# Performance work log

Hardware: AMD Instinct MI355X
Metric: run time of the kernel (lower is better)

The kernel has to match this reference:

```python
import jax, jax.numpy as jnp
import numpy as np

N, E, B = 20000, 200000, 16
ND, ED, GD, HD, DOF = 64, 32, 32, 128, 6
PI = 3.14159265358979

def _hat(v):
    x, y, z = v[..., 0], v[..., 1], v[..., 2]
    O = jnp.zeros_like(x)
    return jnp.stack([jnp.stack([O, -z, y], -1),
                      jnp.stack([z, O, -x], -1),
                      jnp.stack([-y, x, O], -1)], -2)

def _so3_exp(phi):
    th2 = jnp.sum(phi * phi, -1, keepdims=True)
    th = jnp.sqrt(th2 + 1e-12)
    a = jnp.where(th < 1e-4, 1.0 - th2 / 6.0, jnp.sin(th) / th)
    b = jnp.where(th < 1e-4, 0.5 - th2 / 24.0, (1.0 - jnp.cos(th)) / th2)
    K = _hat(phi)
    I = jnp.eye(3, dtype=phi.dtype)
    return I + a[..., None] * K + b[..., None] * (K @ K)

def _se3_exp(rho, phi):
    # returns (R, t) of Exp([rho, phi]) with rotation part phi
    th2 = jnp.sum(phi * phi, -1, keepdims=True)
    th = jnp.sqrt(th2 + 1e-12)
    a = jnp.where(th < 1e-4, 1.0 - th2 / 6.0, jnp.sin(th) / th)
    b = jnp.where(th < 1e-4, 0.5 - th2 / 24.0, (1.0 - jnp.cos(th)) / th2)
    c = jnp.where(th < 1e-4, 1.0 / 6.0 - th2 / 120.0, (th - jnp.sin(th)) / (th2 * th))
    K = _hat(phi)
    KK = K @ K
    I = jnp.eye(3, dtype=phi.dtype)
    R = I + a[..., None] * K + b[..., None] * KK
    V = I + b[..., None] * K + c[..., None] * KK
    t = jnp.einsum('nij,nj->ni', V, rho)
    return R, t

def _comp(Ra, ta, Rb, tb):
    return Ra @ Rb, jnp.einsum('nij,nj->ni', Ra, tb) + ta

def _inv(R, t):
    Rt = jnp.swapaxes(R, -1, -2)
    return Rt, -jnp.einsum('nij,nj->ni', Rt, t)

def _vec(R, t):
    # flattened [R | t] 3x4 -> 12
    return jnp.concatenate([R, t[..., None]], -1).reshape(R.shape[0], 12)

def setup_inputs() -> dict:
    key = jax.random.key(0)
    ks = jax.random.split(key, 16)
    T_R = _so3_exp(0.5 * jax.random.normal(ks[0], (N, 3)))
    Tij_R = _so3_exp(0.5 * jax.random.normal(ks[1], (E, 3)))
    return {
        'xfeat': jax.random.normal(ks[2], (N, ND), jnp.float32),
        'T_R': T_R.astype(jnp.float32),
        'T_t': jax.random.normal(ks[3], (N, 3), jnp.float32),
        'edge_feat': jax.random.normal(ks[4], (E, ED), jnp.float32),
        'Tij_R': Tij_R.astype(jnp.float32),
        'Tij_t': jax.random.normal(ks[5], (E, 3), jnp.float32),
        'u': jax.random.normal(ks[6], (B, GD), jnp.float32),
        'edge_index': jax.random.randint(ks[7], (2, E), 0, N),
        'batch': jnp.sort(jax.random.randint(ks[8], (N,), 0, B)),
        'W1': 0.05 * jax.random.normal(ks[9], (2 * ND + 12 + ED, HD), jnp.float32),
        'b1': jnp.zeros((HD,), jnp.float32),
        'W2': 0.05 * jax.random.normal(ks[10], (HD, HD), jnp.float32),
        'b2': jnp.zeros((HD,), jnp.float32),
        'W3': 0.05 * jax.random.normal(ks[11], (HD + GD + ND, HD), jnp.float32),
        'b3': jnp.zeros((HD,), jnp.float32),
        'W4': 0.05 * jax.random.normal(ks[12], (HD, ND + DOF), jnp.float32),
        'b4': jnp.zeros((ND + DOF,), jnp.float32),
    }

def reference(xfeat, T_R, T_t, edge_feat, Tij_R, Tij_t, u,
              edge_index, batch, W1, b1, W2, b2, W3, b3, W4, b4):
    n = xfeat.shape[0]
    i, j = edge_index[0], edge_index[1]
    xfi, xfj = xfeat[i], xfeat[j]
    Ri, ti = T_R[i], T_t[i]
    Rj, tj = T_R[j], T_t[j]
    # T_err_ij = Tj * Ti.inv() * Tij_hat.inv()
    Rii, tii = _inv(Ri, ti)
    Ra, ta = _comp(Rj, tj, Rii, tii)
    Rhi, thi = _inv(Tij_R, Tij_t)
    Reij, teij = _comp(Ra, ta, Rhi, thi)
    # T_err_ji = Ti * Tj.inv() * Tij_hat
    Rji_, tji_ = _inv(Rj, tj)
    Rb, tb = _comp(Ri, ti, Rji_, tji_)
    Reji, teji = _comp(Rb, tb, Tij_R, Tij_t)
    f_ij = jnp.concatenate([xfi, xfj, edge_feat, _vec(Reij, teij)], 1)
    f_ji = jnp.concatenate([xfj, xfi, edge_feat, _vec(Reji, teji)], 1)
    feats = jnp.concatenate([f_ij, f_ji], 0)          # [2E, 172]
    j_both = jnp.concatenate([j, i], 0)               # [2E]
    h = jax.nn.relu(feats @ W1 + b1)
    h = jax.nn.relu(h @ W2 + b2)                      # [2E, HD]
    sums = jax.ops.segment_sum(h, j_both, num_segments=n)
    cnt = jax.ops.segment_sum(jnp.ones((h.shape[0], 1), h.dtype), j_both, num_segments=n)
    aggr = sums / jnp.maximum(cnt, 1.0)               # scatter_mean
    g = jnp.concatenate([aggr, xfeat, u[batch]], 1)
    out = jax.nn.relu(g @ W3 + b3) @ W4 + b4
    xupd, tupd = out[:, :-DOF], out[:, -DOF:]
    rho, phi = tupd[:, :3], tupd[:, 3:]
    # SquashRot: bound rotation angle to pi via tanh
    th = jnp.linalg.norm(phi, axis=-1, keepdims=True)
    phi = phi * (PI * jnp.tanh(th / PI) / (th + 1e-8))
    Rd, td = _se3_exp(rho, phi)
    R_out, t_out = _comp(Rd, td, T_R, T_t)            # boxplus_left: Exp(d) * T
    xfeat_out = xfeat + xupd
    theta = jnp.linalg.norm(phi, axis=-1, keepdims=True)
    return jnp.concatenate([xfeat_out, R_out.reshape(n, 9), t_out, theta], -1)
```

## Files before the change

kernel.cpp:

```cpp
#include <hip/hip_runtime.h>
#include <math.h>

#define ND 64
#define ED 32
#define GD 32
#define HD 128
#define DOF 6
#define K1 172
#define K1PAD 192
#define KG 224
#define N4P 80
#define NOUT 70
#define OUTC 77
#define MT 256
#define P1 132
#define TDN 16
#define GP 232
#define HP 136
#define OP 84
#define SCB 2048
#define PI_F 3.14159265358979f

typedef short short8 __attribute__((ext_vector_type(8)));
typedef float f32x4  __attribute__((ext_vector_type(4)));

__device__ __forceinline__ unsigned short f2b(float f) {
    unsigned int u = __float_as_uint(f);
    u += 0x7fffu + ((u >> 16) & 1u);
    return (unsigned short)(u >> 16);
}
__device__ __forceinline__ float b2f(unsigned short b) {
    return __uint_as_float(((unsigned int)b) << 16);
}
__device__ __forceinline__ void mul33_abt(const float* A, const float* B, float* C) {
#pragma unroll
    for (int r = 0; r < 3; r++)
#pragma unroll
        for (int c = 0; c < 3; c++)
            C[3*r+c] = A[3*r+0]*B[3*c+0] + A[3*r+1]*B[3*c+1] + A[3*r+2]*B[3*c+2];
}

__global__ void __launch_bounds__(256)
prep(const float* __restrict__ W1, const float* __restrict__ W2,
     const float* __restrict__ W3, const float* __restrict__ W4,
     const float* __restrict__ xfeat, const float* __restrict__ edge_feat,
     const int* __restrict__ edge_index,
     unsigned short* __restrict__ W1b, unsigned short* __restrict__ W2b,
     unsigned short* __restrict__ W3b, unsigned short* __restrict__ W4b,
     unsigned short* __restrict__ xb, unsigned short* __restrict__ eb,
     int* __restrict__ cnti, int N, int E)
{
    int idx = blockIdx.x * 256 + threadIdx.x;
    if (idx < K1PAD * HD) {
        int k = idx >> 7, n = idx & 127;
        float v = (k < K1) ? W1[k * HD + n] : 0.f;
        int kc = k >> 5, kr = k & 31, q = kr >> 3, j = kr & 7;
        W1b[(((kc * 8 + (n >> 4)) * 4 + q) * 16 + (n & 15)) * 8 + j] = f2b(v);
        return;
    }
    idx -= K1PAD * HD;
    if (idx < HD * HD) {
        int k = idx >> 7, n = idx & 127;
        int kc = k >> 5, kr = k & 31, q = kr >> 3, j = kr & 7;
        W2b[(((kc * 8 + (n >> 4)) * 4 + q) * 16 + (n & 15)) * 8 + j] = f2b(W2[k * HD + n]);
        return;
    }
    idx -= HD * HD;
    if (idx < KG * HD) {
        int k = idx >> 7, n = idx & 127;
        int sk = (k < HD) ? ((k & 7) * 16 + (k >> 3)) : k;
        int kc = k >> 5, kr = k & 31, q = kr >> 3, j = kr & 7;
        W3b[(((kc * 8 + (n >> 4)) * 4 + q) * 16 + (n & 15)) * 8 + j] = f2b(W3[sk * HD + n]);
        return;
    }
    idx -= KG * HD;
    if (idx < HD * N4P) {
        int k = idx / N4P, n = idx % N4P;
        float v = (n < NOUT) ? W4[k * NOUT + n] : 0.f;
        int kc = k >> 5, kr = k & 31, q = kr >> 3, j = kr & 7;
        W4b[(((kc * 5 + (n >> 4)) * 4 + q) * 16 + (n & 15)) * 8 + j] = f2b(v);
        return;
    }
    idx -= HD * N4P;
    const int nx4 = N * ND / 4;
    if (idx < nx4) {
        const float4 v = *(const float4*)&xfeat[idx * 4];
        ushort4 o; o.x = f2b(v.x); o.y = f2b(v.y); o.z = f2b(v.z); o.w = f2b(v.w);
        *(ushort4*)&xb[idx * 4] = o;
        return;
    }
    idx -= nx4;
    const int ne4 = E * ED / 4;
    if (idx < ne4) {
        const float4 v = *(const float4*)&edge_feat[idx * 4];
        ushort4 o; o.x = f2b(v.x); o.y = f2b(v.y); o.z = f2b(v.z); o.w = f2b(v.w);
        *(ushort4*)&eb[idx * 4] = o;
        return;
    }
    idx -= ne4;
    if (idx < 2 * E) {
        const int tgt = (idx < E) ? edge_index[E + idx] : edge_index[idx - E];
        atomicAdd(&cnti[tgt], 1);
    }
}

__global__ void __launch_bounds__(256)
scan1(const int* __restrict__ cnti, int* __restrict__ off, int* __restrict__ btot, int N)
{
    __shared__ int sh[SCB];
    __shared__ int tsum[256];
    const int t = threadIdx.x;
    const int base = blockIdx.x * SCB;
    for (int i = t; i < SCB; i += 256) { int g = base + i; sh[i] = (g < N) ? cnti[g] : 0; }
    __syncthreads();
    int loc[8], s = 0;
#pragma unroll
    for (int k = 0; k < 8; k++) { loc[k] = s; s += sh[t * 8 + k]; }
    tsum[t] = s;
    __syncthreads();
    for (int d = 1; d < 256; d <<= 1) {
        int v = (t >= d) ? tsum[t - d] : 0;
        __syncthreads();
        tsum[t] += v;
        __syncthreads();
    }
    const int pre = (t > 0) ? tsum[t - 1] : 0;
#pragma unroll
    for (int k = 0; k < 8; k++) { int g = base + t * 8 + k; if (g < N) off[g] = pre + loc[k]; }
    if (t == 255) btot[blockIdx.x] = tsum[255];
}
__global__ void __launch_bounds__(64)
scan2(int* __restrict__ btot, int nb)
{
    if (threadIdx.x == 0) {
        int s = 0;
        for (int b = 0; b < nb; b++) { int c = btot[b]; btot[b] = s; s += c; }
    }
}
__global__ void __launch_bounds__(256)
scan3(int* __restrict__ off, const int* __restrict__ btot, int* __restrict__ cursor, int N)
{
    int i = blockIdx.x * 256 + threadIdx.x;
    if (i < N) { int v = off[i] + btot[i / SCB]; off[i] = v; cursor[i] = v; }
}

__global__ void __launch_bounds__(256)
scatter_pose(const float* __restrict__ T_R, const float* __restrict__ T_t,
             const float* __restrict__ Tij_R, const float* __restrict__ Tij_t,
             const int* __restrict__ edge_index, int* __restrict__ cursor,
             int4* __restrict__ dinfo, unsigned short* __restrict__ poseb, int E)
{
    const int g = blockIdx.x * 256 + threadIdx.x;
    if (g >= 2 * E) return;
    const bool fwd = (g < E);
    const int e = fwd ? g : g - E;
    const int ni = edge_index[e];
    const int nj = edge_index[E + e];
    const int tgt = fwd ? nj : ni;
    const int pos = atomicAdd(&cursor[tgt], 1);
    dinfo[pos] = make_int4(fwd ? ni : nj, fwd ? nj : ni, e, g);

    float Ri[9], Rj[9], TR[9], ti[3], tj[3], Tt[3];
#pragma unroll
    for (int q = 0; q < 9; q++) { Ri[q] = T_R[9*ni+q]; Rj[q] = T_R[9*nj+q]; TR[q] = Tij_R[9*e+q]; }
#pragma unroll
    for (int q = 0; q < 3; q++) { ti[q] = T_t[3*ni+q]; tj[q] = T_t[3*nj+q]; Tt[q] = Tij_t[3*e+q]; }
    float A[9];
    mul33_abt(Rj, Ri, A);
    float Re[9], te[3];
    if (fwd) {
        mul33_abt(A, TR, Re);
#pragma unroll
        for (int r = 0; r < 3; r++)
            te[r] = tj[r]
                  - (A[3*r+0]*ti[0] + A[3*r+1]*ti[1] + A[3*r+2]*ti[2])
                  - (Re[3*r+0]*Tt[0] + Re[3*r+1]*Tt[1] + Re[3*r+2]*Tt[2]);
    } else {
#pragma unroll
        for (int r = 0; r < 3; r++)
#pragma unroll
            for (int c = 0; c < 3; c++)
                Re[3*r+c] = A[r]*TR[c] + A[3+r]*TR[3+c] + A[6+r]*TR[6+c];
        const float d0 = Tt[0]-tj[0], d1 = Tt[1]-tj[1], d2 = Tt[2]-tj[2];
#pragma unroll
        for (int r = 0; r < 3; r++)
            te[r] = ti[r] + A[r]*d0 + A[3+r]*d1 + A[6+r]*d2;
    }
    short8 p0, p1;
#pragma unroll
    for (int r = 0; r < 2; r++) {
        p0[4*r+0] = (short)f2b(Re[3*r+0]);
        p0[4*r+1] = (short)f2b(Re[3*r+1]);
        p0[4*r+2] = (short)f2b(Re[3*r+2]);
        p0[4*r+3] = (short)f2b(te[r]);
    }
    p1[0] = (short)f2b(Re[6]); p1[1] = (short)f2b(Re[7]);
    p1[2] = (short)f2b(Re[8]); p1[3] = (short)f2b(te[2]);
    p1[4] = 0; p1[5] = 0; p1[6] = 0; p1[7] = 0;
    *(short8*)(poseb + (size_t)pos * 16) = p0;
    *(short8*)(poseb + (size_t)pos * 16 + 8) = p1;
}

__global__ void __launch_bounds__(256, 2)
edge_kernel(const unsigned short* __restrict__ xb, const unsigned short* __restrict__ eb,
            const unsigned short* __restrict__ poseb, const int4* __restrict__ dinfo,
            const unsigned short* __restrict__ W1b, const float* __restrict__ b1,
            const unsigned short* __restrict__ W2b, const float* __restrict__ b2,
            unsigned short* __restrict__ hbuf, int E)
{
    __shared__ unsigned short h1s[4 * 64 * P1];
    const int tid = threadIdx.x;
    const int wv = tid >> 6, lane = tid & 63;
    const int nl = lane & 15, quad = lane >> 4;
    const int D0 = blockIdx.x * MT + wv * 64;
    const int laneoff = quad * 128 + nl * 8;
    const int twoE = 2 * E;
    unsigned short* hw = h1s + wv * 64 * P1;

    int s1[4], s2[4], ee[4], pp[4];
#pragma unroll
    for (int rt = 0; rt < 4; rt++) {
        int p = D0 + rt * 16 + nl;
        if (p >= twoE) p = twoE - 1;
        pp[rt] = p;
        const int4 di = dinfo[p];
        s1[rt] = di.x; s2[rt] = di.y; ee[rt] = di.z;
    }

    f32x4 acc[4][8];
#pragma unroll
    for (int rt = 0; rt < 4; rt++)
#pragma unroll
        for (int At = 0; At < 8; At++) acc[rt][At] = (f32x4)0.f;

    short8 af[2][4], wf[2][8];
#pragma unroll
    for (int rt = 0; rt < 4; rt++)
        af[0][rt] = *(const short8*)(xb + (size_t)s1[rt] * ND + quad * 8);
#pragma unroll
    for (int nt = 0; nt < 8; nt++)
        wf[0][nt] = *(const short8*)(W1b + nt * 512 + laneoff);

#pragma unroll
    for (int kc = 0; kc < 6; kc++) {
        const int cur = kc & 1, nxt = cur ^ 1;
        if (kc < 5) {
#pragma unroll
            for (int rt = 0; rt < 4; rt++) {
                switch (kc + 1) {
                case 1: af[nxt][rt] = *(const short8*)(xb + (size_t)s1[rt] * ND + 32 + quad * 8); break;
                case 2: af[nxt][rt] = *(const short8*)(xb + (size_t)s2[rt] * ND + quad * 8); break;
                case 3: af[nxt][rt] = *(const short8*)(xb + (size_t)s2[rt] * ND + 32 + quad * 8); break;
                case 4: af[nxt][rt] = *(const short8*)(eb + (size_t)ee[rt] * ED + quad * 8); break;
                default: af[nxt][rt] = (quad < 2) ? *(const short8*)(poseb + (size_t)pp[rt] * 16 + quad * 8)
                                                  : (short8)(short)0; break;
                }
            }
#pragma unroll
            for (int nt = 0; nt < 8; nt++)
                wf[nxt][nt] = *(const short8*)(W1b + ((kc + 1) * 8 + nt) * 512 + laneoff);
        }
#pragma unroll
        for (int At = 0; At < 8; At++)
#pragma unroll
            for (int rt = 0; rt < 4; rt++)
                acc[rt][At] = __builtin_amdgcn_mfma_f32_16x16x32_bf16(wf[cur][At], af[cur][rt], acc[rt][At], 0, 0, 0);
    }

#pragma unroll
    for (int At = 0; At < 8; At++) {
        const f32x4 bv = *(const f32x4*)&b1[At * 16 + quad * 4];
#pragma unroll
        for (int rt = 0; rt < 4; rt++) {
            unsigned int lo = (unsigned int)f2b(fmaxf(acc[rt][At][0] + bv[0], 0.f))
                            | ((unsigned int)f2b(fmaxf(acc[rt][At][1] + bv[1], 0.f)) << 16);
            unsigned int hi = (unsigned int)f2b(fmaxf(acc[rt][At][2] + bv[2], 0.f))
                            | ((unsigned int)f2b(fmaxf(acc[rt][At][3] + bv[3], 0.f)) << 16);
            uint2 pk; pk.x = lo; pk.y = hi;
            *(uint2*)&hw[(rt * 16 + nl) * P1 + At * 16 + quad * 4] = pk;
        }
    }
    asm volatile("s_waitcnt lgkmcnt(0)" ::: "memory");

#pragma unroll
    for (int rt = 0; rt < 4; rt++)
#pragma unroll
        for (int nt = 0; nt < 8; nt++) acc[rt][nt] = (f32x4)0.f;
#pragma unroll
    for (int nt = 0; nt < 8; nt++)
        wf[0][nt] = *(const short8*)(W2b + nt * 512 + laneoff);
#pragma unroll
    for (int kc = 0; kc < 4; kc++) {
        union { short8 s; uint2 u[2]; } hf[4];
#pragma unroll
        for (int rt = 0; rt < 4; rt++) {
            const unsigned short* hp = &hw[(rt * 16 + nl) * P1 + kc * 32 + quad * 8];
            hf[rt].u[0] = *(const uint2*)hp;
            hf[rt].u[1] = *(const uint2*)(hp + 4);
        }
        const int cur = kc & 1, nxt = cur ^ 1;
        if (kc < 3) {
#pragma unroll
            for (int nt = 0; nt < 8; nt++)
                wf[nxt][nt] = *(const short8*)(W2b + ((kc + 1) * 8 + nt) * 512 + laneoff);
        }
#pragma unroll
        for (int nt = 0; nt < 8; nt++)
#pragma unroll
            for (int rt = 0; rt < 4; rt++)
                acc[rt][nt] = __builtin_amdgcn_mfma_f32_16x16x32_bf16(hf[rt].s, wf[cur][nt], acc[rt][nt], 0, 0, 0);
    }

    {
        float bias2[8];
#pragma unroll
        for (int nt = 0; nt < 8; nt++) bias2[nt] = b2[nt * 16 + nl];
#pragma unroll
        for (int rt = 0; rt < 4; rt++)
#pragma unroll
            for (int r = 0; r < 4; r++) {
                const int p2 = D0 + rt * 16 + quad * 4 + r;
                if (p2 < twoE) {
                    short8 hv;
#pragma unroll
                    for (int nt = 0; nt < 8; nt++)
                        hv[nt] = (short)f2b(fmaxf(acc[rt][nt][r] + bias2[nt], 0.f));
                    *(short8*)(hbuf + (size_t)p2 * HD + nl * 8) = hv;
                }
            }
    }
}

__global__ void __launch_bounds__(256)
node_kernel(const float* __restrict__ xfeat, const float* __restrict__ T_R,
            const float* __restrict__ T_t, const float* __restrict__ u,
            const int* __restrict__ batch,
            const unsigned short* __restrict__ W3b, const float* __restrict__ b3,
            const unsigned short* __restrict__ W4b, const float* __restrict__ b4,
            const unsigned short* __restrict__ hbuf, const int* __restrict__ off,
            const int* __restrict__ cnti,
            float* __restrict__ out, int Nn)
{
    __shared__ unsigned short gbuf[TDN * GP];
    __shared__ unsigned short hid[TDN * HP];
    __shared__ float obuf[TDN * OP];
    const int tid = threadIdx.x;
    const int wv = tid >> 6, lane = tid & 63;
    const int n0 = blockIdx.x * TDN;
    const int nn = min(TDN, Nn - n0);

#pragma unroll
    for (int i = 0; i < 4; i++) {
        const int d = wv + 4 * i;
        if (d < nn) {
            const int n = n0 + d;
            const int deg = cnti[n];
            const int start = off[n];
            const float inv = 1.0f / (float)max(deg, 1);
            const unsigned short* hp = hbuf + (size_t)start * HD + 2 * lane;
            float a0 = 0.f, a1 = 0.f;
            int k = 0;
            for (; k + 4 <= deg; k += 4) {
                const unsigned int v0 = *(const unsigned int*)(hp);
                const unsigned int v1 = *(const unsigned int*)(hp + HD);
                const unsigned int v2 = *(const unsigned int*)(hp + 2 * HD);
                const unsigned int v3 = *(const unsigned int*)(hp + 3 * HD);
                hp += 4 * HD;
                a0 += b2f((unsigned short)v0) + b2f((unsigned short)v1)
                    + b2f((unsigned short)v2) + b2f((unsigned short)v3);
                a1 += b2f((unsigned short)(v0 >> 16)) + b2f((unsigned short)(v1 >> 16))
                    + b2f((unsigned short)(v2 >> 16)) + b2f((unsigned short)(v3 >> 16));
            }
            for (; k < deg; k++) {
                const unsigned int v0 = *(const unsigned int*)(hp);
                hp += HD;
                a0 += b2f((unsigned short)v0);
                a1 += b2f((unsigned short)(v0 >> 16));
            }
            const unsigned int pk = (unsigned int)f2b(a0 * inv) | ((unsigned int)f2b(a1 * inv) << 16);
            *(unsigned int*)&gbuf[d * GP + 2 * lane] = pk;
        }
    }
    for (int idx = tid; idx < TDN * 24; idx += 256) {
        const int d = idx / 24;
        if (d < nn) {
            const int n = n0 + d;
            const int c4 = (idx % 24) * 4;
            float4 v;
            if (c4 < 64) v = *(const float4*)&xfeat[(size_t)n * ND + c4];
            else         v = *(const float4*)&u[(size_t)batch[n] * GD + (c4 - 64)];
            ushort4 o; o.x = f2b(v.x); o.y = f2b(v.y); o.z = f2b(v.z); o.w = f2b(v.w);
            *(ushort4*)&gbuf[d * GP + 128 + c4] = o;
        }
    }
    __syncthreads();

    const int nl = lane & 15, quad = lane >> 4;
    const int laneoff = quad * 128 + nl * 8;

    f32x4 acc3[2];
    acc3[0] = (f32x4)0.f; acc3[1] = (f32x4)0.f;
#pragma unroll
    for (int kc = 0; kc < 7; kc++) {
        short8 A0 = *(const short8*)&gbuf[nl * GP + kc * 32 + quad * 8];
#pragma unroll
        for (int t = 0; t < 2; t++) {
            short8 B = *(const short8*)(W3b + (kc * 8 + wv * 2 + t) * 512 + laneoff);
            acc3[t] = __builtin_amdgcn_mfma_f32_16x16x32_bf16(A0, B, acc3[t], 0, 0, 0);
        }
    }
#pragma unroll
    for (int t = 0; t < 2; t++) {
        const int col = (wv * 2 + t) * 16 + nl;
        const float bb = b3[col];
#pragma unroll
        for (int r = 0; r < 4; r++)
            hid[(quad * 4 + r) * HP + col] = f2b(fmaxf(acc3[t][r] + bb, 0.f));
    }
    __syncthreads();

    f32x4 acc4[2];
    acc4[0] = (f32x4)0.f; acc4[1] = (f32x4)0.f;
    const int nt1 = (wv == 0) ? 4 : -1;
#pragma unroll
    for (int kc = 0; kc < 4; kc++) {
        short8 A0 = *(const short8*)&hid[nl * HP + kc * 32 + quad * 8];
        short8 B0 = *(const short8*)(W4b + (kc * 5 + wv) * 512 + laneoff);
        acc4[0] = __builtin_amdgcn_mfma_f32_16x16x32_bf16(A0, B0, acc4[0], 0, 0, 0);
        if (nt1 >= 0) {
            short8 B1 = *(const short8*)(W4b + (kc * 5 + nt1) * 512 + laneoff);
            acc4[1] = __builtin_amdgcn_mfma_f32_16x16x32_bf16(A0, B1, acc4[1], 0, 0, 0);
        }
    }
    {
        const int col0 = wv * 16 + nl;
        const float bb0 = (col0 < NOUT) ? b4[col0] : 0.f;
#pragma unroll
        for (int r = 0; r < 4; r++)
            obuf[(quad * 4 + r) * OP + col0] = acc4[0][r] + bb0;
        if (nt1 >= 0) {
            const int col1 = nt1 * 16 + nl;
            const float bb1 = (col1 < NOUT) ? b4[col1] : 0.f;
#pragma unroll
            for (int r = 0; r < 4; r++)
                obuf[(quad * 4 + r) * OP + col1] = acc4[1][r] + bb1;
        }
    }
    __syncthreads();

    for (int idx = tid; idx < TDN * ND; idx += 256) {
        const int d = idx >> 6, c = idx & 63;
        if (d < nn) {
            const int n = n0 + d;
            out[(size_t)n * OUTC + c] = xfeat[(size_t)n * ND + c] + obuf[d * OP + c];
        }
    }
    if (tid < nn) {
        const int n = n0 + tid;
        const float r0 = obuf[tid*OP + 64], r1 = obuf[tid*OP + 65], r2 = obuf[tid*OP + 66];
        float p0 = obuf[tid*OP + 67], p1 = obuf[tid*OP + 68], p2 = obuf[tid*OP + 69];
        const float th0 = sqrtf(p0*p0 + p1*p1 + p2*p2);
        const float s = PI_F * tanhf(th0 / PI_F) / (th0 + 1e-8f);
        p0 *= s; p1 *= s; p2 *= s;
        const float pp = p0*p0 + p1*p1 + p2*p2;
        const float th = sqrtf(pp + 1e-12f);
        float a, b, c;
        if (th < 1e-4f) { a = 1.f - pp/6.f; b = 0.5f - pp/24.f; c = 1.f/6.f - pp/120.f; }
        else { const float sn = sinf(th), cs = cosf(th); a = sn/th; b = (1.f-cs)/pp; c = (th-sn)/(pp*th); }
        float Rd[9], V[9];
        Rd[0]=1.f+b*(p0*p0-pp); Rd[1]=-a*p2+b*p0*p1; Rd[2]= a*p1+b*p0*p2;
        Rd[3]= a*p2+b*p1*p0;    Rd[4]=1.f+b*(p1*p1-pp); Rd[5]=-a*p0+b*p1*p2;
        Rd[6]=-a*p1+b*p2*p0;    Rd[7]= a*p0+b*p2*p1;  Rd[8]=1.f+b*(p2*p2-pp);
        V[0]=1.f+c*(p0*p0-pp);  V[1]=-b*p2+c*p0*p1;   V[2]= b*p1+c*p0*p2;
        V[3]= b*p2+c*p1*p0;     V[4]=1.f+c*(p1*p1-pp); V[5]=-b*p0+c*p1*p2;
        V[6]=-b*p1+c*p2*p0;     V[7]= b*p0+c*p2*p1;   V[8]=1.f+c*(p2*p2-pp);
        const float td0 = V[0]*r0 + V[1]*r1 + V[2]*r2;
        const float td1 = V[3]*r0 + V[4]*r1 + V[5]*r2;
        const float td2 = V[6]*r0 + V[7]*r1 + V[8]*r2;
        float TRn[9], Ttn[3];
#pragma unroll
        for (int q = 0; q < 9; q++) TRn[q] = T_R[9*n+q];
#pragma unroll
        for (int q = 0; q < 3; q++) Ttn[q] = T_t[3*n+q];
        float* o = out + (size_t)n * OUTC + 64;
#pragma unroll
        for (int r = 0; r < 3; r++)
#pragma unroll
            for (int cc = 0; cc < 3; cc++)
                o[3*r+cc] = Rd[3*r+0]*TRn[cc] + Rd[3*r+1]*TRn[3+cc] + Rd[3*r+2]*TRn[6+cc];
        o[9]  = Rd[0]*Ttn[0] + Rd[1]*Ttn[1] + Rd[2]*Ttn[2] + td0;
        o[10] = Rd[3]*Ttn[0] + Rd[4]*Ttn[1] + Rd[5]*Ttn[2] + td1;
        o[11] = Rd[6]*Ttn[0] + Rd[7]*Ttn[1] + Rd[8]*Ttn[2] + td2;
        o[12] = sqrtf(pp);
    }
}

extern "C" void kernel_launch(void* const* d_in, const int* in_sizes, int n_in,
                              void* d_out, int out_size, void* d_ws, size_t ws_size,
                              hipStream_t stream)
{
    const float* xfeat     = (const float*)d_in[0];
    const float* T_R       = (const float*)d_in[1];
    const float* T_t       = (const float*)d_in[2];
    const float* edge_feat = (const float*)d_in[3];
    const float* Tij_R     = (const float*)d_in[4];
    const float* Tij_t     = (const float*)d_in[5];
    const float* u         = (const float*)d_in[6];
    const int*   edge_index= (const int*)d_in[7];
    const int*   batch     = (const int*)d_in[8];
    const float* W1 = (const float*)d_in[9],  *b1 = (const float*)d_in[10];
    const float* W2 = (const float*)d_in[11], *b2 = (const float*)d_in[12];
    const float* W3 = (const float*)d_in[13], *b3 = (const float*)d_in[14];
    const float* W4 = (const float*)d_in[15], *b4 = (const float*)d_in[16];
    const int N = in_sizes[0] / ND;
    const int E = in_sizes[3] / ED;

    char* p = (char*)d_ws;
    unsigned short* W1b = (unsigned short*)p;   p += (size_t)K1PAD * HD * 2;
    unsigned short* W2b = (unsigned short*)p;   p += (size_t)HD * HD * 2;
    unsigned short* W3b = (unsigned short*)p;   p += (size_t)KG * HD * 2;
    unsigned short* W4b = (unsigned short*)p;   p += (size_t)HD * N4P * 2;
    unsigned short* xb  = (unsigned short*)p;   p += (size_t)N * ND * 2;
    unsigned short* ebf = (unsigned short*)p;   p += (size_t)E * ED * 2;
    unsigned short* poseb = (unsigned short*)p; p += (size_t)2 * E * 16 * 2;
    unsigned short* hbuf = (unsigned short*)p;  p += (size_t)2 * E * HD * 2;
    int4* dinfo = (int4*)p;                     p += (size_t)2 * E * 16;
    int* cnti = (int*)p;                        p += (size_t)N * 4;
    int* off  = (int*)p;                        p += (size_t)N * 4;
    int* cursor = (int*)p;                      p += (size_t)N * 4;
    int* btot = (int*)p;

    hipMemsetAsync(cnti, 0, (size_t)N * 4, stream);
    const int prepn = K1PAD*HD + HD*HD + KG*HD + HD*N4P + N*ND/4 + E*ED/4 + 2*E;
    prep<<<(prepn + 255) / 256, 256, 0, stream>>>(W1, W2, W3, W4, xfeat, edge_feat,
                                                  edge_index, W1b, W2b, W3b, W4b,
                                                  xb, ebf, cnti, N, E);
    const int nsb = (N + SCB - 1) / SCB;
    scan1<<<nsb, 256, 0, stream>>>(cnti, off, btot, N);
    scan2<<<1, 64, 0, stream>>>(btot, nsb);
    scan3<<<(N + 255) / 256, 256, 0, stream>>>(off, btot, cursor, N);
    scatter_pose<<<(2*E + 255) / 256, 256, 0, stream>>>(T_R, T_t, Tij_R, Tij_t,
                                                        edge_index, cursor, dinfo, poseb, E);
    const int ebk = (2 * E + MT - 1) / MT;
    edge_kernel<<<ebk, 256, 0, stream>>>(xb, ebf, poseb, dinfo,
                                         W1b, b1, W2b, b2, hbuf, E);
    const int nb = (N + TDN - 1) / TDN;
    node_kernel<<<nb, 256, 0, stream>>>(xfeat, T_R, T_t, u, batch, W3b, b3, W4b, b4,
                                        hbuf, off, cnti, (float*)d_out, N);
}
```

Measured before the change: 265.6 us.

## Split scatter from pose computation and vectorize node aggregation loads

The fused scatter_pose kernel is split in two. A light scatter kernel writes only edge ids into a destination-sorted list, and a separate pose kernel reads that list and writes dinfo and the pose records at consecutive positions, so those stores are coalesced instead of going to scattered atomic positions. Node aggregation now has each lane load 8 bf16 values (16 bytes) across 4 row groups and combines them with cross-lane shuffles, replacing the old 4-byte-per-lane loads. The cost is an extra kernel launch, an extra list buffer, and gathered rather than sequential reads of edge_index and poses in the pose kernel.

```diff
diff --git a/kernel.cpp b/kernel.cpp
--- a/kernel.cpp
+++ b/kernel.cpp
@@ -145,20 +145,30 @@
 }
 
 __global__ void __launch_bounds__(256)
-scatter_pose(const float* __restrict__ T_R, const float* __restrict__ T_t,
-             const float* __restrict__ Tij_R, const float* __restrict__ Tij_t,
-             const int* __restrict__ edge_index, int* __restrict__ cursor,
-             int4* __restrict__ dinfo, unsigned short* __restrict__ poseb, int E)
-{
-    const int g = blockIdx.x * 256 + threadIdx.x;
+scatter_kernel(const int* __restrict__ edge_index, int* __restrict__ cursor,
+               int* __restrict__ dlist, int E)
+{
+    int g = blockIdx.x * 256 + threadIdx.x;
     if (g >= 2 * E) return;
+    const int tgt = (g < E) ? edge_index[E + g] : edge_index[g - E];
+    const int pos = atomicAdd(&cursor[tgt], 1);
+    dlist[pos] = g;
+}
+
+__global__ void __launch_bounds__(256)
+pose_kernel(const float* __restrict__ T_R, const float* __restrict__ T_t,
+            const float* __restrict__ Tij_R, const float* __restrict__ Tij_t,
+            const int* __restrict__ edge_index, const int* __restrict__ dlist,
+            int4* __restrict__ dinfo, unsigned short* __restrict__ poseb, int E)
+{
+    const int p = blockIdx.x * 256 + threadIdx.x;
+    if (p >= 2 * E) return;
+    const int g = dlist[p];
     const bool fwd = (g < E);
     const int e = fwd ? g : g - E;
     const int ni = edge_index[e];
     const int nj = edge_index[E + e];
-    const int tgt = fwd ? nj : ni;
-    const int pos = atomicAdd(&cursor[tgt], 1);
-    dinfo[pos] = make_int4(fwd ? ni : nj, fwd ? nj : ni, e, g);
+    dinfo[p] = make_int4(fwd ? ni : nj, fwd ? nj : ni, e, g);
 
     float Ri[9], Rj[9], TR[9], ti[3], tj[3], Tt[3];
 #pragma unroll
@@ -197,8 +207,8 @@
     p1[0] = (short)f2b(Re[6]); p1[1] = (short)f2b(Re[7]);
     p1[2] = (short)f2b(Re[8]); p1[3] = (short)f2b(te[2]);
     p1[4] = 0; p1[5] = 0; p1[6] = 0; p1[7] = 0;
-    *(short8*)(poseb + (size_t)pos * 16) = p0;
-    *(short8*)(poseb + (size_t)pos * 16 + 8) = p1;
+    *(short8*)(poseb + (size_t)p * 16) = p0;
+    *(short8*)(poseb + (size_t)p * 16 + 8) = p1;
 }
 
 __global__ void __launch_bounds__(256, 2)
@@ -349,6 +359,8 @@
     const int n0 = blockIdx.x * TDN;
     const int nn = min(TDN, Nn - n0);
 
+    const int cg = lane & 15;
+    const int rq = lane >> 4;
 #pragma unroll
     for (int i = 0; i < 4; i++) {
         const int d = wv + 4 * i;
@@ -357,28 +369,26 @@
             const int deg = cnti[n];
             const int start = off[n];
             const float inv = 1.0f / (float)max(deg, 1);
-            const unsigned short* hp = hbuf + (size_t)start * HD + 2 * lane;
-            float a0 = 0.f, a1 = 0.f;
-            int k = 0;
-            for (; k + 4 <= deg; k += 4) {
-                const unsigned int v0 = *(const unsigned int*)(hp);
-                const unsigned int v1 = *(const unsigned int*)(hp + HD);
-                const unsigned int v2 = *(const unsigned int*)(hp + 2 * HD);
-                const unsigned int v3 = *(const unsigned int*)(hp + 3 * HD);
-                hp += 4 * HD;
-                a0 += b2f((unsigned short)v0) + b2f((unsigned short)v1)
-                    + b2f((unsigned short)v2) + b2f((unsigned short)v3);
-                a1 += b2f((unsigned short)(v0 >> 16)) + b2f((unsigned short)(v1 >> 16))
-                    + b2f((unsigned short)(v2 >> 16)) + b2f((unsigned short)(v3 >> 16));
+            const unsigned short* base = hbuf + (size_t)start * HD + cg * 8;
+            float facc[8];
+#pragma unroll
+            for (int j = 0; j < 8; j++) facc[j] = 0.f;
+            for (int r = rq; r < deg; r += 4) {
+                const short8 v = *(const short8*)(base + (size_t)r * HD);
+#pragma unroll
+                for (int j = 0; j < 8; j++) facc[j] += b2f((unsigned short)v[j]);
             }
-            for (; k < deg; k++) {
-                const unsigned int v0 = *(const unsigned int*)(hp);
-                hp += HD;
-                a0 += b2f((unsigned short)v0);
-                a1 += b2f((unsigned short)(v0 >> 16));
+#pragma unroll
+            for (int j = 0; j < 8; j++) {
+                facc[j] += __shfl_xor(facc[j], 16);
+                facc[j] += __shfl_xor(facc[j], 32);
             }
-            const unsigned int pk = (unsigned int)f2b(a0 * inv) | ((unsigned int)f2b(a1 * inv) << 16);
-            *(unsigned int*)&gbuf[d * GP + 2 * lane] = pk;
+            if (rq == 0) {
+                short8 o;
+#pragma unroll
+                for (int j = 0; j < 8; j++) o[j] = (short)f2b(facc[j] * inv);
+                *(short8*)&gbuf[d * GP + cg * 8] = o;
+            }
         }
     }
     for (int idx = tid; idx < TDN * 24; idx += 256) {
@@ -525,6 +535,7 @@
     unsigned short* poseb = (unsigned short*)p; p += (size_t)2 * E * 16 * 2;
     unsigned short* hbuf = (unsigned short*)p;  p += (size_t)2 * E * HD * 2;
     int4* dinfo = (int4*)p;                     p += (size_t)2 * E * 16;
+    int* dlist = (int*)p;                       p += (size_t)2 * E * 4;
     int* cnti = (int*)p;                        p += (size_t)N * 4;
     int* off  = (int*)p;                        p += (size_t)N * 4;
     int* cursor = (int*)p;                      p += (size_t)N * 4;
@@ -539,8 +550,9 @@
     scan1<<<nsb, 256, 0, stream>>>(cnti, off, btot, N);
     scan2<<<1, 64, 0, stream>>>(btot, nsb);
     scan3<<<(N + 255) / 256, 256, 0, stream>>>(off, btot, cursor, N);
-    scatter_pose<<<(2*E + 255) / 256, 256, 0, stream>>>(T_R, T_t, Tij_R, Tij_t,
-                                                        edge_index, cursor, dinfo, poseb, E);
+    scatter_kernel<<<(2*E + 255) / 256, 256, 0, stream>>>(edge_index, cursor, dlist, E);
+    pose_kernel<<<(2*E + 255) / 256, 256, 0, stream>>>(T_R, T_t, Tij_R, Tij_t,
+                                                       edge_index, dlist, dinfo, poseb, E);
     const int ebk = (2 * E + MT - 1) / MT;
     edge_kernel<<<ebk, 256, 0, stream>>>(xb, ebf, poseb, dinfo,
                                          W1b, b1, W2b, b2, hbuf, E);
```

New measurement: 286.3 us. 1.08x slower.
